# Performance work log

Hardware: AMD Instinct MI355X
Metric: run time of the kernel (lower is better)

The kernel has to match this reference:

```python
import jax, jax.numpy as jnp
import numpy as np

INV_PI = 0.31830988618
PI_over_2 = 1.57079632679
PI_over_4 = 0.78539816339
N_MODES, DIM, COND_C = 8, 2, 64
LAYERS = [COND_C, 128, 512, 128, 32, N_MODES * DIM * 2 + N_MODES + 1]
N = 262144


def setup_inputs() -> dict:
    key = jax.random.key(0)
    ks = jax.random.split(key, 2 + 2 * (len(LAYERS) - 1))
    inp = {}
    inp["cond_vec"] = jax.random.normal(ks[0], (N, COND_C), jnp.float32)
    # uniforms in (0,1), bounded away from 0/1 so log/div are finite
    inp["randseed"] = jax.random.uniform(ks[1], (N, 2), jnp.float32, 1e-4, 1.0 - 1e-4)
    for i in range(len(LAYERS) - 1):
        inp[f"W{i}"] = jax.random.normal(ks[2 + 2 * i], (LAYERS[i], LAYERS[i + 1]), jnp.float32) * 0.01
        inp[f"b{i}"] = jnp.zeros((LAYERS[i + 1],), jnp.float32)
    return inp


def _mlp(x, Ws, bs):
    for i, (W, b) in enumerate(zip(Ws, bs)):
        x = x @ W + b
        if i < len(Ws) - 1:
            x = jax.nn.relu(x)
    return x


def _forward(cond_vec, randseed, Ws, bs):
    nm, d = N_MODES, DIM
    h = _mlp(cond_vec, Ws, bs)  # [N, nm*d*2 + nm + 1]
    loc = h[:, : nm * d].reshape(-1, nm, d)
    log_scale = h[:, nm * d : 2 * nm * d].reshape(-1, nm, d)
    w = jnp.abs(h[:, 2 * nm * d :])
    w = w / jnp.sum(w, axis=1, keepdims=True)  # [N, nm+1]
    wL = w[:, -1]

    r0, r1 = randseed[:, 0], randseed[:, 1]
    lambert_mask = r0 < wL
    gauss_mask = ~lambert_mask
    # in-place rescale of randseed column 0 in the torch code
    u0 = jnp.where(lambert_mask, r0 / wL, (r0 - wL) / (1.0 - wL))

    # --- gauss branch (Box-Muller) ---
    U1 = jnp.where(gauss_mask, u0, 0.5)  # masked positions: safe dummy
    U1 = jnp.maximum(U1, 1e-12)
    R = jnp.sqrt(-2.0 * jnp.log(U1))
    th = 2.0 * jnp.pi * r1
    eps_ = jnp.stack([R * jnp.cos(th), R * jnp.sin(th)], axis=-1)  # [N, 2]
    scale_sample = jnp.sum(jnp.exp(log_scale), axis=1)  # [N, 2]
    loc_sample = jnp.sum(loc, axis=1)  # [N, 2]
    z_gauss = eps_ * scale_sample + loc_sample

    # --- lambert branch (concentric disk map) ---
    wo0 = u0 * 2.0 - 1.0
    wo1 = r1 * 2.0 - 1.0
    nonzero = ~((wo0 == 0) & (wo1 == 0))
    cond1 = (jnp.abs(wo0) > jnp.abs(wo1)) & nonzero
    cond2 = (~cond1) & nonzero
    safe0 = jnp.where(wo0 == 0, 1.0, wo0)
    safe1 = jnp.where(wo1 == 0, 1.0, wo1)
    phi = jnp.where(cond1, PI_over_4 * wo1 / safe0, PI_over_2 - PI_over_4 * wo0 / safe1)
    r = jnp.where(cond1, wo0, jnp.where(cond2, wo1, 0.0))
    z_lambert = jnp.stack([r * jnp.cos(phi), r * jnp.sin(phi)], axis=-1)

    z = jnp.where(lambert_mask[:, None], z_lambert, z_gauss)  # [N, 2]

    # --- mixture log prob ---
    eps = (z[:, None, :] - loc) / jnp.exp(log_scale)  # [N, nm, 2]
    log_p = (-0.5 * d * jnp.log(2.0 * jnp.pi)
             + jnp.log(w[:, :-1] + 1e-5)
             - 0.5 * jnp.sum(eps ** 2, axis=2)
             - jnp.sum(log_scale, axis=2))  # [N, nm]
    pdf = jnp.where(z[:, 0] ** 2 + z[:, 1] ** 2 > 1.0, 0.0, INV_PI)
    lambert_log_p = jnp.log(pdf + 1e-5) + jnp.log(wL)
    log_p = jnp.concatenate([log_p, lambert_log_p[:, None]], axis=-1)  # [N, nm+1]
    return z, jax.scipy.special.logsumexp(log_p, axis=1)


def reference(cond_vec, randseed, W0, b0, W1, b1, W2, b2, W3, b3, W4, b4):
    Ws = [W0, W1, W2, W3, W4]
    bs = [b0, b1, b2, b3, b4]
    return _forward(cond_vec, randseed, Ws, bs)
```

## Files before the change

### kernel.cpp

```cpp
#include <hip/hip_runtime.h>
#include <math.h>

#define NTOT   262144
#define ROWS   64
#define THREADS 512
#define KB     16

__global__ __launch_bounds__(THREADS, 4)
void gmm_fused(const float* __restrict__ cond,
               const float* __restrict__ rnd,
               const float* __restrict__ W0, const float* __restrict__ b0,
               const float* __restrict__ W1, const float* __restrict__ b1,
               const float* __restrict__ W2, const float* __restrict__ b2,
               const float* __restrict__ W3, const float* __restrict__ b3,
               const float* __restrict__ W4, const float* __restrict__ b4,
               float* __restrict__ out)
{
    extern __shared__ float smem[];
    float* Bs0 = smem;
    float* Bs1 = smem + 128 * 64;

    const int tid  = threadIdx.x;
    const int lane = tid & 63;
    const int wv   = tid >> 6;
    const int row0 = blockIdx.x * ROWS;

    {
        const float4* cond4 = (const float4*)cond;
        #pragma unroll
        for (int p = 0; p < 2; ++p) {
            int i  = p * THREADS + tid;
            int r  = i & 63;
            int c4 = i >> 6;
            float4 v = cond4[(size_t)(row0 + r) * 16 + c4];
            Bs0[(4 * c4 + 0) * 64 + r] = v.x;
            Bs0[(4 * c4 + 1) * 64 + r] = v.y;
            Bs0[(4 * c4 + 2) * 64 + r] = v.z;
            Bs0[(4 * c4 + 3) * 64 + r] = v.w;
        }
    }
    __syncthreads();

    const int wc16 = __builtin_amdgcn_readfirstlane(wv * 16);

    {
        float acc[16];
        #pragma unroll
        for (int c = 0; c < 16; ++c) acc[c] = b0[wc16 + c];
        for (int kb = 0; kb < 64; kb += KB) {
            float a[KB];
            #pragma unroll
            for (int kk = 0; kk < KB; ++kk) a[kk] = Bs0[(kb + kk) * 64 + lane];
            #pragma unroll
            for (int kk = 0; kk < KB; ++kk) {
                const float* wr = W0 + (kb + kk) * 128 + wc16;
                #pragma unroll
                for (int c = 0; c < 16; ++c) acc[c] = fmaf(a[kk], wr[c], acc[c]);
            }
        }
        #pragma unroll
        for (int c = 0; c < 16; ++c)
            Bs1[(wc16 + c) * 64 + lane] = fmaxf(acc[c], 0.0f);
    }
    __syncthreads();

    float acc2[16];
    #pragma unroll
    for (int c = 0; c < 16; ++c) acc2[c] = b2[wc16 + c];

    for (int chunk = 0; chunk < 4; ++chunk) {
        float t[16];
        const int cb = chunk * 128 + wc16;
        #pragma unroll
        for (int c = 0; c < 16; ++c) t[c] = b1[cb + c];

        for (int kb = 0; kb < 128; kb += KB) {
            float a[KB];
            #pragma unroll
            for (int kk = 0; kk < KB; ++kk) a[kk] = Bs1[(kb + kk) * 64 + lane];
            #pragma unroll
            for (int kk = 0; kk < KB; ++kk) {
                const float* wr = W1 + (size_t)(kb + kk) * 512 + cb;
                #pragma unroll
                for (int c = 0; c < 16; ++c) t[c] = fmaf(a[kk], wr[c], t[c]);
            }
        }
        __syncthreads();
        #pragma unroll
        for (int c = 0; c < 16; ++c)
            Bs0[(wc16 + c) * 64 + lane] = fmaxf(t[c], 0.0f);
        __syncthreads();

        for (int kb = 0; kb < 128; kb += KB) {
            float a[KB];
            #pragma unroll
            for (int kk = 0; kk < KB; ++kk) a[kk] = Bs0[(kb + kk) * 64 + lane];
            #pragma unroll
            for (int kk = 0; kk < KB; ++kk) {
                const float* wr = W2 + (size_t)(chunk * 128 + kb + kk) * 128 + wc16;
                #pragma unroll
                for (int c = 0; c < 16; ++c) acc2[c] = fmaf(a[kk], wr[c], acc2[c]);
            }
        }
    }
    #pragma unroll
    for (int c = 0; c < 16; ++c)
        Bs1[(wc16 + c) * 64 + lane] = fmaxf(acc2[c], 0.0f);
    __syncthreads();

    const int wc4 = __builtin_amdgcn_readfirstlane(wv * 4);
    {
        float acc[4];
        #pragma unroll
        for (int c = 0; c < 4; ++c) acc[c] = b3[wc4 + c];
        for (int kb = 0; kb < 128; kb += KB) {
            float a[KB];
            #pragma unroll
            for (int kk = 0; kk < KB; ++kk) a[kk] = Bs1[(kb + kk) * 64 + lane];
            #pragma unroll
            for (int kk = 0; kk < KB; ++kk) {
                const float* wr = W3 + (kb + kk) * 32 + wc4;
                #pragma unroll
                for (int c = 0; c < 4; ++c) acc[c] = fmaf(a[kk], wr[c], acc[c]);
            }
        }
        #pragma unroll
        for (int c = 0; c < 4; ++c)
            Bs0[(wc4 + c) * 64 + lane] = fmaxf(acc[c], 0.0f);
    }
    __syncthreads();

    const int wc6 = __builtin_amdgcn_readfirstlane(wv * 6);
    {
        float acc[6];
        #pragma unroll
        for (int c = 0; c < 6; ++c) acc[c] = (wc6 + c < 41) ? b4[wc6 + c] : 0.0f;
        {
            float a[32];
            #pragma unroll
            for (int kk = 0; kk < 32; ++kk) a[kk] = Bs0[kk * 64 + lane];
            #pragma unroll
            for (int kk = 0; kk < 32; ++kk) {
                const float* wr = W4 + kk * 41;
                #pragma unroll
                for (int c = 0; c < 6; ++c)
                    if (wc6 + c < 41) acc[c] = fmaf(a[kk], wr[wc6 + c], acc[c]);
            }
        }
        #pragma unroll
        for (int c = 0; c < 6; ++c)
            if (wc6 + c < 41) Bs1[(wc6 + c) * 64 + lane] = acc[c];
    }
    __syncthreads();

    if (wv == 0) {
        const int row = row0 + lane;
        float h[41];
        #pragma unroll
        for (int j = 0; j < 41; ++j) h[j] = Bs1[j * 64 + lane];

        float2 rv = ((const float2*)rnd)[row];
        float r0v = rv.x, r1v = rv.y;

        float wraw[9];
        float wsum = 0.0f;
        #pragma unroll
        for (int j = 0; j < 9; ++j) { wraw[j] = fabsf(h[32 + j]); wsum += wraw[j]; }
        float wL = wraw[8] / wsum;

        const bool lambert = r0v < wL;
        float u0 = lambert ? (r0v / wL) : ((r0v - wL) / (1.0f - wL));
        float U1 = lambert ? 0.5f : u0;
        U1 = fmaxf(U1, 1e-12f);
        float R  = sqrtf(-2.0f * logf(U1));
        float th = 6.28318530717958647692f * r1v;
        float ce = cosf(th), se = sinf(th);

        float es0[8], es1[8];
        float ssum0 = 0.0f, ssum1 = 0.0f, lsum0 = 0.0f, lsum1 = 0.0f;
        #pragma unroll
        for (int m = 0; m < 8; ++m) {
            es0[m] = expf(h[16 + 2 * m]);
            es1[m] = expf(h[16 + 2 * m + 1]);
            ssum0 += es0[m]; ssum1 += es1[m];
            lsum0 += h[2 * m]; lsum1 += h[2 * m + 1];
        }
        float zg0 = (R * ce) * ssum0 + lsum0;
        float zg1 = (R * se) * ssum1 + lsum1;

        float wo0 = u0 * 2.0f - 1.0f;
        float wo1 = r1v * 2.0f - 1.0f;
        bool nonzero = !((wo0 == 0.0f) && (wo1 == 0.0f));
        bool c1 = (fabsf(wo0) > fabsf(wo1)) && nonzero;
        bool c2 = (!c1) && nonzero;
        float sa0 = (wo0 == 0.0f) ? 1.0f : wo0;
        float sa1 = (wo1 == 0.0f) ? 1.0f : wo1;
        float phi = c1 ? (0.78539816339f * wo1 / sa0)
                       : (1.57079632679f - 0.78539816339f * wo0 / sa1);
        float rr = c1 ? wo0 : (c2 ? wo1 : 0.0f);
        float zl0 = rr * cosf(phi);
        float zl1 = rr * sinf(phi);

        float z0 = lambert ? zl0 : zg0;
        float z1 = lambert ? zl1 : zg1;

        float lp[9];
        #pragma unroll
        for (int m = 0; m < 8; ++m) {
            float e0 = (z0 - h[2 * m])     / es0[m];
            float e1 = (z1 - h[2 * m + 1]) / es1[m];
            float wm = wraw[m] / wsum;
            lp[m] = (-1.83787706640934548356f + logf(wm + 1e-5f))
                    - 0.5f * (e0 * e0 + e1 * e1)
                    - (h[16 + 2 * m] + h[16 + 2 * m + 1]);
        }
        float pdf = (z0 * z0 + z1 * z1 > 1.0f) ? 0.0f : 0.31830988618f;
        lp[8] = logf(pdf + 1e-5f) + logf(wL);

        float mx = lp[0];
        #pragma unroll
        for (int j = 1; j < 9; ++j) mx = fmaxf(mx, lp[j]);
        float s = 0.0f;
        #pragma unroll
        for (int j = 0; j < 9; ++j) s += expf(lp[j] - mx);
        float lse = mx + logf(s);

        ((float2*)out)[row] = make_float2(z0, z1);
        out[(size_t)2 * NTOT + row] = lse;
    }
}

extern "C" void kernel_launch(void* const* d_in, const int* in_sizes, int n_in,
                              void* d_out, int out_size, void* d_ws, size_t ws_size,
                              hipStream_t stream) {
    const float* cond = (const float*)d_in[0];
    const float* rnd  = (const float*)d_in[1];
    const float* W0 = (const float*)d_in[2];  const float* b0 = (const float*)d_in[3];
    const float* W1 = (const float*)d_in[4];  const float* b1 = (const float*)d_in[5];
    const float* W2 = (const float*)d_in[6];  const float* b2 = (const float*)d_in[7];
    const float* W3 = (const float*)d_in[8];  const float* b3 = (const float*)d_in[9];
    const float* W4 = (const float*)d_in[10]; const float* b4 = (const float*)d_in[11];
    float* out = (float*)d_out;

    dim3 grid(NTOT / ROWS);
    dim3 block(THREADS);
    size_t shmem = (size_t)2 * 128 * 64 * sizeof(float);
    hipLaunchKernelGGL(gmm_fused, grid, block, shmem, stream,
                       cond, rnd, W0, b0, W1, b1, W2, b2, W3, b3, W4, b4, out);
}
```

Measured before the change: 996.5 us.

## Process two rows per lane and shrink layer-1 chunking to cut weight reloads

Each block now covers 128 rows, and every lane computes two rows using float2 LDS reads. Each weight value, which arrives as a wave-uniform scalar load, is therefore reused for two FMAs. The 512-wide hidden layer is now split into 16 chunks of 32 columns instead of 4 of 128, so the intermediate buffer needs less shared memory. The cost is more accumulator registers, more barriers per block and fewer blocks in the grid.

```diff
diff --git a/kernel.cpp b/kernel.cpp
--- a/kernel.cpp
+++ b/kernel.cpp
@@ -1,10 +1,10 @@
 #include <hip/hip_runtime.h>
 #include <math.h>
 
-#define NTOT   262144
-#define ROWS   64
+#define NTOT    262144
+#define ROWS    128
 #define THREADS 512
-#define KB     16
+#define KB      8
 
 __global__ __launch_bounds__(THREADS, 4)
 void gmm_fused(const float* __restrict__ cond,
@@ -17,147 +17,183 @@
                float* __restrict__ out)
 {
     extern __shared__ float smem[];
-    float* Bs0 = smem;
-    float* Bs1 = smem + 128 * 64;
+    float* BsA = smem;
+    float* BsC = smem + 128 * 128;
 
     const int tid  = threadIdx.x;
     const int lane = tid & 63;
     const int wv   = tid >> 6;
     const int row0 = blockIdx.x * ROWS;
+    const int r2   = 2 * lane;
 
     {
         const float4* cond4 = (const float4*)cond;
         #pragma unroll
-        for (int p = 0; p < 2; ++p) {
+        for (int p = 0; p < 4; ++p) {
             int i  = p * THREADS + tid;
-            int r  = i & 63;
-            int c4 = i >> 6;
+            int r  = i & 127;
+            int c4 = i >> 7;
             float4 v = cond4[(size_t)(row0 + r) * 16 + c4];
-            Bs0[(4 * c4 + 0) * 64 + r] = v.x;
-            Bs0[(4 * c4 + 1) * 64 + r] = v.y;
-            Bs0[(4 * c4 + 2) * 64 + r] = v.z;
-            Bs0[(4 * c4 + 3) * 64 + r] = v.w;
+            BsA[(4 * c4 + 0) * 128 + r] = v.x;
+            BsA[(4 * c4 + 1) * 128 + r] = v.y;
+            BsA[(4 * c4 + 2) * 128 + r] = v.z;
+            BsA[(4 * c4 + 3) * 128 + r] = v.w;
         }
     }
     __syncthreads();
 
     const int wc16 = __builtin_amdgcn_readfirstlane(wv * 16);
-
-    {
-        float acc[16];
-        #pragma unroll
-        for (int c = 0; c < 16; ++c) acc[c] = b0[wc16 + c];
+    const int wc4  = __builtin_amdgcn_readfirstlane(wv * 4);
+    const int wc6  = __builtin_amdgcn_readfirstlane(wv * 6);
+
+    {
+        float acc0[16], acc1[16];
+        #pragma unroll
+        for (int c = 0; c < 16; ++c) { acc0[c] = b0[wc16 + c]; acc1[c] = acc0[c]; }
         for (int kb = 0; kb < 64; kb += KB) {
-            float a[KB];
-            #pragma unroll
-            for (int kk = 0; kk < KB; ++kk) a[kk] = Bs0[(kb + kk) * 64 + lane];
+            float2 a[KB];
+            #pragma unroll
+            for (int kk = 0; kk < KB; ++kk)
+                a[kk] = *(const float2*)&BsA[(kb + kk) * 128 + r2];
             #pragma unroll
             for (int kk = 0; kk < KB; ++kk) {
                 const float* wr = W0 + (kb + kk) * 128 + wc16;
                 #pragma unroll
-                for (int c = 0; c < 16; ++c) acc[c] = fmaf(a[kk], wr[c], acc[c]);
-            }
-        }
+                for (int c = 0; c < 16; ++c) {
+                    float w = wr[c];
+                    acc0[c] = fmaf(a[kk].x, w, acc0[c]);
+                    acc1[c] = fmaf(a[kk].y, w, acc1[c]);
+                }
+            }
+        }
+        __syncthreads();
         #pragma unroll
         for (int c = 0; c < 16; ++c)
-            Bs1[(wc16 + c) * 64 + lane] = fmaxf(acc[c], 0.0f);
-    }
-    __syncthreads();
-
-    float acc2[16];
+            *(float2*)&BsA[(wc16 + c) * 128 + r2] =
+                make_float2(fmaxf(acc0[c], 0.0f), fmaxf(acc1[c], 0.0f));
+    }
+    __syncthreads();
+
+    float acc20[16], acc21[16];
     #pragma unroll
-    for (int c = 0; c < 16; ++c) acc2[c] = b2[wc16 + c];
-
-    for (int chunk = 0; chunk < 4; ++chunk) {
-        float t[16];
-        const int cb = chunk * 128 + wc16;
-        #pragma unroll
-        for (int c = 0; c < 16; ++c) t[c] = b1[cb + c];
+    for (int c = 0; c < 16; ++c) { acc20[c] = b2[wc16 + c]; acc21[c] = acc20[c]; }
+
+    for (int chunk = 0; chunk < 16; ++chunk) {
+        const int cb = chunk * 32 + wc4;
+        float t0[4], t1[4];
+        #pragma unroll
+        for (int c = 0; c < 4; ++c) { t0[c] = b1[cb + c]; t1[c] = t0[c]; }
 
         for (int kb = 0; kb < 128; kb += KB) {
-            float a[KB];
-            #pragma unroll
-            for (int kk = 0; kk < KB; ++kk) a[kk] = Bs1[(kb + kk) * 64 + lane];
+            float2 a[KB];
+            #pragma unroll
+            for (int kk = 0; kk < KB; ++kk)
+                a[kk] = *(const float2*)&BsA[(kb + kk) * 128 + r2];
             #pragma unroll
             for (int kk = 0; kk < KB; ++kk) {
                 const float* wr = W1 + (size_t)(kb + kk) * 512 + cb;
                 #pragma unroll
-                for (int c = 0; c < 16; ++c) t[c] = fmaf(a[kk], wr[c], t[c]);
+                for (int c = 0; c < 4; ++c) {
+                    float w = wr[c];
+                    t0[c] = fmaf(a[kk].x, w, t0[c]);
+                    t1[c] = fmaf(a[kk].y, w, t1[c]);
+                }
             }
         }
         __syncthreads();
         #pragma unroll
-        for (int c = 0; c < 16; ++c)
-            Bs0[(wc16 + c) * 64 + lane] = fmaxf(t[c], 0.0f);
+        for (int c = 0; c < 4; ++c)
+            *(float2*)&BsC[(wc4 + c) * 128 + r2] =
+                make_float2(fmaxf(t0[c], 0.0f), fmaxf(t1[c], 0.0f));
         __syncthreads();
 
-        for (int kb = 0; kb < 128; kb += KB) {
-            float a[KB];
-            #pragma unroll
-            for (int kk = 0; kk < KB; ++kk) a[kk] = Bs0[(kb + kk) * 64 + lane];
-            #pragma unroll
-            for (int kk = 0; kk < KB; ++kk) {
-                const float* wr = W2 + (size_t)(chunk * 128 + kb + kk) * 128 + wc16;
-                #pragma unroll
-                for (int c = 0; c < 16; ++c) acc2[c] = fmaf(a[kk], wr[c], acc2[c]);
+        for (int kb = 0; kb < 32; kb += KB) {
+            float2 a[KB];
+            #pragma unroll
+            for (int kk = 0; kk < KB; ++kk)
+                a[kk] = *(const float2*)&BsC[(kb + kk) * 128 + r2];
+            #pragma unroll
+            for (int kk = 0; kk < KB; ++kk) {
+                const float* wr = W2 + (size_t)(chunk * 32 + kb + kk) * 128 + wc16;
+                #pragma unroll
+                for (int c = 0; c < 16; ++c) {
+                    float w = wr[c];
+                    acc20[c] = fmaf(a[kk].x, w, acc20[c]);
+                    acc21[c] = fmaf(a[kk].y, w, acc21[c]);
+                }
             }
         }
     }
     #pragma unroll
     for (int c = 0; c < 16; ++c)
-        Bs1[(wc16 + c) * 64 + lane] = fmaxf(acc2[c], 0.0f);
-    __syncthreads();
-
-    const int wc4 = __builtin_amdgcn_readfirstlane(wv * 4);
-    {
-        float acc[4];
-        #pragma unroll
-        for (int c = 0; c < 4; ++c) acc[c] = b3[wc4 + c];
+        *(float2*)&BsA[(wc16 + c) * 128 + r2] =
+            make_float2(fmaxf(acc20[c], 0.0f), fmaxf(acc21[c], 0.0f));
+    __syncthreads();
+
+    {
+        float a30[4], a31[4];
+        #pragma unroll
+        for (int c = 0; c < 4; ++c) { a30[c] = b3[wc4 + c]; a31[c] = a30[c]; }
         for (int kb = 0; kb < 128; kb += KB) {
-            float a[KB];
-            #pragma unroll
-            for (int kk = 0; kk < KB; ++kk) a[kk] = Bs1[(kb + kk) * 64 + lane];
+            float2 a[KB];
+            #pragma unroll
+            for (int kk = 0; kk < KB; ++kk)
+                a[kk] = *(const float2*)&BsA[(kb + kk) * 128 + r2];
             #pragma unroll
             for (int kk = 0; kk < KB; ++kk) {
                 const float* wr = W3 + (kb + kk) * 32 + wc4;
                 #pragma unroll
-                for (int c = 0; c < 4; ++c) acc[c] = fmaf(a[kk], wr[c], acc[c]);
+                for (int c = 0; c < 4; ++c) {
+                    float w = wr[c];
+                    a30[c] = fmaf(a[kk].x, w, a30[c]);
+                    a31[c] = fmaf(a[kk].y, w, a31[c]);
+                }
             }
         }
         #pragma unroll
         for (int c = 0; c < 4; ++c)
-            Bs0[(wc4 + c) * 64 + lane] = fmaxf(acc[c], 0.0f);
-    }
-    __syncthreads();
-
-    const int wc6 = __builtin_amdgcn_readfirstlane(wv * 6);
-    {
-        float acc[6];
-        #pragma unroll
-        for (int c = 0; c < 6; ++c) acc[c] = (wc6 + c < 41) ? b4[wc6 + c] : 0.0f;
-        {
-            float a[32];
-            #pragma unroll
-            for (int kk = 0; kk < 32; ++kk) a[kk] = Bs0[kk * 64 + lane];
-            #pragma unroll
-            for (int kk = 0; kk < 32; ++kk) {
-                const float* wr = W4 + kk * 41;
+            *(float2*)&BsC[(wc4 + c) * 128 + r2] =
+                make_float2(fmaxf(a30[c], 0.0f), fmaxf(a31[c], 0.0f));
+    }
+    __syncthreads();
+
+    {
+        float a40[6], a41[6];
+        #pragma unroll
+        for (int c = 0; c < 6; ++c) {
+            float b = (wc6 + c < 41) ? b4[wc6 + c] : 0.0f;
+            a40[c] = b; a41[c] = b;
+        }
+        for (int kb = 0; kb < 32; kb += KB) {
+            float2 a[KB];
+            #pragma unroll
+            for (int kk = 0; kk < KB; ++kk)
+                a[kk] = *(const float2*)&BsC[(kb + kk) * 128 + r2];
+            #pragma unroll
+            for (int kk = 0; kk < KB; ++kk) {
+                const float* wr = W4 + (kb + kk) * 41;
                 #pragma unroll
                 for (int c = 0; c < 6; ++c)
-                    if (wc6 + c < 41) acc[c] = fmaf(a[kk], wr[wc6 + c], acc[c]);
+                    if (wc6 + c < 41) {
+                        float w = wr[wc6 + c];
+                        a40[c] = fmaf(a[kk].x, w, a40[c]);
+                        a41[c] = fmaf(a[kk].y, w, a41[c]);
+                    }
             }
         }
         #pragma unroll
         for (int c = 0; c < 6; ++c)
-            if (wc6 + c < 41) Bs1[(wc6 + c) * 64 + lane] = acc[c];
-    }
-    __syncthreads();
-
-    if (wv == 0) {
-        const int row = row0 + lane;
+            if (wc6 + c < 41)
+                *(float2*)&BsA[(wc6 + c) * 128 + r2] = make_float2(a40[c], a41[c]);
+    }
+    __syncthreads();
+
+    if (tid < 128) {
+        const int e   = tid;
+        const int row = row0 + e;
         float h[41];
         #pragma unroll
-        for (int j = 0; j < 41; ++j) h[j] = Bs1[j * 64 + lane];
+        for (int j = 0; j < 41; ++j) h[j] = BsA[j * 128 + e];
 
         float2 rv = ((const float2*)rnd)[row];
         float r0v = rv.x, r1v = rv.y;
@@ -244,7 +280,7 @@
 
     dim3 grid(NTOT / ROWS);
     dim3 block(THREADS);
-    size_t shmem = (size_t)2 * 128 * 64 * sizeof(float);
+    size_t shmem = (size_t)(128 * 128 + 32 * 128) * sizeof(float);
     hipLaunchKernelGGL(gmm_fused, grid, block, shmem, stream,
                        cond, rnd, W0, b0, W1, b1, W2, b2, W3, b3, W4, b4, out);
 }
```

Measured after the change: 984.3 us. Within noise of the previous version (-1.2%).
